# Performance work log

Measured on AMD Instinct MI355X. Metric: run time of the kernel, lower is better.

The kernel has to match this reference:

```python
import jax, jax.numpy as jnp
import numpy as np

NUM_ITERATIONS = 3


def squash(s, axis=-1):
    # s * sqrt(||s||^2) / (1 + ||s||^2), matching the torch source exactly
    sq = jnp.sum(s * s, axis=axis, keepdims=True)
    return s * jnp.sqrt(sq) / (1.0 + sq)


def setup_inputs() -> dict:
    key = jax.random.key(0)
    k_u, k_w = jax.random.split(key)
    B, J, R, O, I = 128, 166, 864, 8, 4
    u = jax.random.normal(k_u, (B, R, I), dtype=jnp.float32)
    W = jax.random.normal(k_w, (1, J, R, O, I), dtype=jnp.float32)
    return {"u": u, "W": W}


def reference(u, W):
    # u: [B, R, I]; W: [1, J, R, O, I]
    Wq = W[0]  # [J, R, O, I]
    # u_hat[b,j,r,o] = sum_i W[j,r,o,i] * u[b,r,i]
    u_hat = jnp.einsum('jroi,bri->bjro', Wq, u)  # [B, J, R, O]
    # routing logits start shared across batch (torch init: [1,J,R,1,1])
    b_ij = jnp.zeros((1, Wq.shape[0], Wq.shape[1]), dtype=u_hat.dtype)  # [1, J, R]
    v_j = None
    for it in range(NUM_ITERATIONS):
        c_ij = jax.nn.softmax(b_ij, axis=2)           # softmax over routes R
        s_j = jnp.einsum('bjr,bjro->bjo', jnp.broadcast_to(c_ij, u_hat.shape[:3]), u_hat)  # [B, J, O]
        v_j = squash(s_j, axis=-1)                    # [B, J, O]
        if it < NUM_ITERATIONS - 1:
            # agreement a[b,j,r] = <u_hat[b,j,r,:], v[b,j,:]>
            a_ij = jnp.einsum('bjro,bjo->bjr', u_hat, v_j)
            b_ij = b_ij + a_ij                        # broadcasts to [B, J, R]
    return v_j  # equivalent to torch v_j.squeeze() for B > 1
```

## Files before the change

### kernel.cpp

```cpp
#include <hip/hip_runtime.h>
#include <math.h>


#define BB 128
#define JJ 166
#define RR 864
#define OO 8
#define KMAX 14
#define RPAD2 257

typedef __fp16 h2v __attribute__((ext_vector_type(2)));

__device__ __forceinline__ uint32_t pack2(float a, float b) {
    return __builtin_bit_cast(uint32_t, __builtin_amdgcn_cvt_pkrtz(a, b));
}
__device__ __forceinline__ h2v bc_h2(uint32_t u) {
    return __builtin_bit_cast(h2v, u);
}
__device__ __forceinline__ float lo_f(uint32_t u) {
    return (float)__builtin_bit_cast(h2v, u).x;
}
__device__ __forceinline__ float hi_f(uint32_t u) {
    return (float)__builtin_bit_cast(h2v, u).y;
}

__device__ __forceinline__ float wave_sum(float v) {
#pragma unroll
    for (int m = 32; m >= 1; m >>= 1) v += __shfl_xor(v, m, 64);
    return v;
}

__global__ __launch_bounds__(256) void digitcaps_kernel(
    const float* __restrict__ u, const float* __restrict__ W,
    float* __restrict__ out) {
    const int tid = threadIdx.x;
    const int lane = tid & 63;
    const int wave = tid >> 6;

    const int j = blockIdx.x >> 5;
    const int b = ((blockIdx.x & 31) << 2) + wave;

    const float4* __restrict__ u4 = (const float4*)u;
    const float4* __restrict__ W4 = (const float4*)W;

    __shared__ uint2 wlds[2][OO * RPAD2];

    uint32_t uh[KMAX][4];

#define STAGE(CC, BUF, ITERS)                                                  \
    {                                                                          \
        const int gbase = j * (RR * OO) + (CC * 256) * OO;                     \
        _Pragma("unroll")                                                      \
        for (int i = 0; i < (ITERS); ++i) {                                    \
            const int e = tid + (i << 8);                                      \
            const float4 w = W4[gbase + e];                                    \
            wlds[BUF][(e & 7) * RPAD2 + (e >> 3)] =                            \
                make_uint2(pack2(w.x, w.y), pack2(w.z, w.w));                  \
        }                                                                      \
    }

#define COMPUTE(CC, BUF, KK)                                                   \
    {                                                                          \
        _Pragma("unroll")                                                      \
        for (int kl = 0; kl < (KK); ++kl) {                                    \
            const int rl = (kl << 6) + lane;                                   \
            const int r = (CC * 256) + rl;                                     \
            if (r < RR) {                      \
                const float4 uu = u4[b * RR + r];                              \
                const uint32_t up0 = pack2(uu.x, uu.y);                        \
                const uint32_t up1 = pack2(uu.z, uu.w);                        \
                float d[OO];                                                   \
                _Pragma("unroll")                                              \
                for (int o = 0; o < OO; ++o) {                                 \
                    const uint2 ww = wlds[BUF][o * RPAD2 + rl];                \
                    float t = __builtin_amdgcn_fdot2(bc_h2(ww.x), bc_h2(up0),  \
                                                     0.0f, false);             \
                    d[o] = __builtin_amdgcn_fdot2(bc_h2(ww.y), bc_h2(up1), t,  \
                                                  false);                      \
                }                                                              \
                _Pragma("unroll")                                              \
                for (int o2 = 0; o2 < 4; ++o2)                                 \
                    uh[(CC) * 4 + kl][o2] = pack2(d[2 * o2], d[2 * o2 + 1]);   \
            } else {                                                           \
                _Pragma("unroll")                                              \
                for (int o2 = 0; o2 < 4; ++o2) uh[(CC) * 4 + kl][o2] = 0u;     \
            }                                                                  \
        }                                                                      \
    }

    STAGE(0, 0, 8)
    __syncthreads();
    STAGE(1, 1, 8)
    COMPUTE(0, 0, 4)
    __syncthreads();
    STAGE(2, 0, 8)
    COMPUTE(1, 1, 4)
    __syncthreads();
    STAGE(3, 1, 3)
    COMPUTE(2, 0, 4)
    __syncthreads();
    COMPUTE(3, 1, 2)
#undef STAGE
#undef COMPUTE

    float V[OO];
    float v[OO];

    {
        h2v accp[4];
#pragma unroll
        for (int o2 = 0; o2 < 4; ++o2) accp[o2] = bc_h2(uh[0][o2]);
#pragma unroll
        for (int k = 1; k < KMAX; ++k)
#pragma unroll
            for (int o2 = 0; o2 < 4; ++o2) accp[o2] += bc_h2(uh[k][o2]);

        float s[OO];
#pragma unroll
        for (int o2 = 0; o2 < 4; ++o2) {
            s[2 * o2]     = wave_sum((float)accp[o2].x) * (1.0f / (float)RR);
            s[2 * o2 + 1] = wave_sum((float)accp[o2].y) * (1.0f / (float)RR);
        }
        float n2 = 0.0f;
#pragma unroll
        for (int o = 0; o < OO; ++o) n2 += s[o] * s[o];
        const float scale = sqrtf(n2) / (1.0f + n2);
#pragma unroll
        for (int o = 0; o < OO; ++o) { v[o] = s[o] * scale; V[o] = v[o]; }
    }

#pragma unroll
    for (int it = 1; it < 3; ++it) {
        uint32_t Vp[4];
#pragma unroll
        for (int o2 = 0; o2 < 4; ++o2)
            Vp[o2] = pack2(V[2 * o2], V[2 * o2 + 1]);

        float zp = 0.0f;
        float sp[OO];
#pragma unroll
        for (int o = 0; o < OO; ++o) sp[o] = 0.0f;

#pragma unroll
        for (int k = 0; k < KMAX; ++k) {
            float br = 0.0f;
#pragma unroll
            for (int o2 = 0; o2 < 4; ++o2)
                br = __builtin_amdgcn_fdot2(bc_h2(uh[k][o2]), bc_h2(Vp[o2]),
                                            br, false);
            const float e = (k < KMAX - 1 || lane < 32) ? __expf(br) : 0.0f;
            zp += e;
#pragma unroll
            for (int o2 = 0; o2 < 4; ++o2) {
                sp[2 * o2]     = fmaf(e, lo_f(uh[k][o2]), sp[2 * o2]);
                sp[2 * o2 + 1] = fmaf(e, hi_f(uh[k][o2]), sp[2 * o2 + 1]);
            }
        }
        const float invZ = 1.0f / wave_sum(zp);

        float s[OO];
#pragma unroll
        for (int o = 0; o < OO; ++o) s[o] = wave_sum(sp[o]) * invZ;

        float n2 = 0.0f;
#pragma unroll
        for (int o = 0; o < OO; ++o) n2 += s[o] * s[o];
        const float scale = sqrtf(n2) / (1.0f + n2);
#pragma unroll
        for (int o = 0; o < OO; ++o) v[o] = s[o] * scale;

        if (it < 2) {
#pragma unroll
            for (int o = 0; o < OO; ++o) V[o] += v[o];
        }
    }

    float outv = 0.0f;
#pragma unroll
    for (int o = 0; o < OO; ++o)
        if (lane == o) outv = v[o];
    if (lane < OO) out[(b * JJ + j) * OO + lane] = outv;
}

extern "C" void kernel_launch(void* const* d_in, const int* in_sizes, int n_in,
                              void* d_out, int out_size, void* d_ws, size_t ws_size,
                              hipStream_t stream) {
    const float* u = (const float*)d_in[0];
    const float* W = (const float*)d_in[1];
    float* out = (float*)d_out;

    const int grid = JJ * (BB / 4);
    digitcaps_kernel<<<grid, 256, 0, stream>>>(u, W, out);
}
```

Baseline: 144.0 us.

## Prepack W and u to fp16 in workspace and stream via global_load_lds

Adds a prepack kernel that converts W and u to packed fp16 in workspace, with W stored in an o-major, route-tiled layout and u padded. The main kernel then stages W tiles directly into LDS with global_load_lds, doing no per-block conversion or transpose. It also reads pre-packed u without bounds checks, moves to 512-thread blocks (8 batches per block), and remaps block IDs so neighbouring blocks share j. This removes the redundant per-block fp32 loads and conversions of W, which were repeated 32 times per j, at the cost of an extra kernel launch and a workspace round-trip.

```diff
diff --git a/kernel.cpp b/kernel.cpp
--- a/kernel.cpp
+++ b/kernel.cpp
@@ -7,7 +7,8 @@
 #define RR 864
 #define OO 8
 #define KMAX 14
-#define RPAD2 257
+#define WP_U2 (JJ * 7168)
+#define UP_U2 (BB * 896)
 
 typedef __fp16 h2v __attribute__((ext_vector_type(2)));
 
@@ -30,76 +31,111 @@
     return v;
 }
 
-__global__ __launch_bounds__(256) void digitcaps_kernel(
+__global__ __launch_bounds__(256) void prepack_kernel(
     const float* __restrict__ u, const float* __restrict__ W,
+    uint2* __restrict__ ws) {
+    const int t = threadIdx.x;
+    const int bid = blockIdx.x;
+    if (bid < JJ * 4) {
+        const int j = bid >> 2;
+        const int c = bid & 3;
+        const float4* __restrict__ W4 = (const float4*)W;
+        uint2* __restrict__ dst = ws + (size_t)j * 7168 + c * 2048;
+        if (c < 3) {
+#pragma unroll
+            for (int i = 0; i < 8; ++i) {
+                const int r = c * 256 + t;
+                const float4 w = W4[((size_t)j * RR + r) * 8 + i];
+                dst[i * 256 + t] = make_uint2(pack2(w.x, w.y), pack2(w.z, w.w));
+            }
+        } else {
+#pragma unroll
+            for (int i = 0; i < 4; ++i) {
+                const int e = i * 256 + t;
+                const int o = e >> 7;
+                const int rl = e & 127;
+                float4 w = make_float4(0.f, 0.f, 0.f, 0.f);
+                if (rl < 96) w = W4[((size_t)j * RR + 768 + rl) * 8 + o];
+                dst[e] = make_uint2(pack2(w.x, w.y), pack2(w.z, w.w));
+            }
+        }
+    } else {
+        const int e = (bid - JJ * 4) * 256 + t;
+        const int b = e / 896;
+        const int r = e - b * 896;
+        const float4* __restrict__ u4 = (const float4*)u;
+        float4 uu = make_float4(0.f, 0.f, 0.f, 0.f);
+        if (r < RR) uu = u4[(size_t)b * RR + r];
+        ws[WP_U2 + e] = make_uint2(pack2(uu.x, uu.y), pack2(uu.z, uu.w));
+    }
+}
+
+__global__ __launch_bounds__(512) void digitcaps_kernel(
+    const uint2* __restrict__ Wp, const uint2* __restrict__ uP,
     float* __restrict__ out) {
     const int tid = threadIdx.x;
     const int lane = tid & 63;
     const int wave = tid >> 6;
 
-    const int j = blockIdx.x >> 5;
-    const int b = ((blockIdx.x & 31) << 2) + wave;
-
-    const float4* __restrict__ u4 = (const float4*)u;
-    const float4* __restrict__ W4 = (const float4*)W;
-
-    __shared__ uint2 wlds[2][OO * RPAD2];
+    int bid = blockIdx.x;
+    bid = (bid & 7) * 332 + (bid >> 3);
+    const int j = bid >> 4;
+    const int b = ((bid & 15) << 3) + wave;
+
+    __shared__ uint2 wlds[2][2048];
+
+    const uint2* __restrict__ uPb = uP + (size_t)b * 896;
 
     uint32_t uh[KMAX][4];
 
-#define STAGE(CC, BUF, ITERS)                                                  \
+#define STAGE(CC, BUF, ROUNDS)                                                 \
     {                                                                          \
-        const int gbase = j * (RR * OO) + (CC * 256) * OO;                     \
+        const char* gsrc =                                                     \
+            (const char*)(Wp + (size_t)j * 7168 + (CC) * 2048);                \
         _Pragma("unroll")                                                      \
-        for (int i = 0; i < (ITERS); ++i) {                                    \
-            const int e = tid + (i << 8);                                      \
-            const float4 w = W4[gbase + e];                                    \
-            wlds[BUF][(e & 7) * RPAD2 + (e >> 3)] =                            \
-                make_uint2(pack2(w.x, w.y), pack2(w.z, w.w));                  \
+        for (int i = 0; i < (ROUNDS); ++i) {                                   \
+            __builtin_amdgcn_global_load_lds(                                  \
+                (const __attribute__((address_space(1))) uint32_t*)            \
+                    (gsrc + i * 8192 + tid * 16),                              \
+                (__attribute__((address_space(3))) uint32_t*)                  \
+                    ((char*)(&wlds[BUF][0]) + i * 8192 + (wave << 10)),        \
+                16, 0, 0);                                                     \
         }                                                                      \
     }
 
-#define COMPUTE(CC, BUF, KK)                                                   \
+#define COMPUTE(CC, BUF, KK, STRIDE)                                           \
     {                                                                          \
         _Pragma("unroll")                                                      \
         for (int kl = 0; kl < (KK); ++kl) {                                    \
             const int rl = (kl << 6) + lane;                                   \
-            const int r = (CC * 256) + rl;                                     \
-            if (r < RR) {                      \
-                const float4 uu = u4[b * RR + r];                              \
-                const uint32_t up0 = pack2(uu.x, uu.y);                        \
-                const uint32_t up1 = pack2(uu.z, uu.w);                        \
-                float d[OO];                                                   \
-                _Pragma("unroll")                                              \
-                for (int o = 0; o < OO; ++o) {                                 \
-                    const uint2 ww = wlds[BUF][o * RPAD2 + rl];                \
-                    float t = __builtin_amdgcn_fdot2(bc_h2(ww.x), bc_h2(up0),  \
-                                                     0.0f, false);             \
-                    d[o] = __builtin_amdgcn_fdot2(bc_h2(ww.y), bc_h2(up1), t,  \
-                                                  false);                      \
-                }                                                              \
-                _Pragma("unroll")                                              \
-                for (int o2 = 0; o2 < 4; ++o2)                                 \
-                    uh[(CC) * 4 + kl][o2] = pack2(d[2 * o2], d[2 * o2 + 1]);   \
-            } else {                                                           \
-                _Pragma("unroll")                                              \
-                for (int o2 = 0; o2 < 4; ++o2) uh[(CC) * 4 + kl][o2] = 0u;     \
+            const uint2 up = uPb[(CC) * 256 + rl];                             \
+            float d[OO];                                                       \
+            _Pragma("unroll")                                                  \
+            for (int o = 0; o < OO; ++o) {                                     \
+                const uint2 ww = wlds[BUF][o * (STRIDE) + rl];                 \
+                float t = __builtin_amdgcn_fdot2(bc_h2(ww.x), bc_h2(up.x),     \
+                                                 0.0f, false);                 \
+                d[o] = __builtin_amdgcn_fdot2(bc_h2(ww.y), bc_h2(up.y), t,     \
+                                              false);                          \
             }                                                                  \
+            _Pragma("unroll")                                                  \
+            for (int o2 = 0; o2 < 4; ++o2)                                     \
+                uh[(CC) * 4 + kl][o2] = pack2(d[2 * o2], d[2 * o2 + 1]);       \
         }                                                                      \
     }
 
-    STAGE(0, 0, 8)
-    __syncthreads();
-    STAGE(1, 1, 8)
-    COMPUTE(0, 0, 4)
-    __syncthreads();
-    STAGE(2, 0, 8)
-    COMPUTE(1, 1, 4)
-    __syncthreads();
-    STAGE(3, 1, 3)
-    COMPUTE(2, 0, 4)
-    __syncthreads();
-    COMPUTE(3, 1, 2)
+    STAGE(0, 0, 2)
+    __syncthreads();
+    STAGE(1, 1, 2)
+    COMPUTE(0, 0, 4, 256)
+    __syncthreads();
+    STAGE(2, 0, 2)
+    COMPUTE(1, 1, 4, 256)
+    __syncthreads();
+    STAGE(3, 1, 1)
+    COMPUTE(2, 0, 4, 256)
+    __syncthreads();
+    COMPUTE(3, 1, 2, 128)
 #undef STAGE
 #undef COMPUTE
 
@@ -188,7 +224,9 @@
     const float* u = (const float*)d_in[0];
     const float* W = (const float*)d_in[1];
     float* out = (float*)d_out;
-
-    const int grid = JJ * (BB / 4);
-    digitcaps_kernel<<<grid, 256, 0, stream>>>(u, W, out);
-}
+    uint2* ws = (uint2*)d_ws;
+
+    prepack_kernel<<<JJ * 4 + (BB * 896) / 256, 256, 0, stream>>>(u, W, ws);
+
+    digitcaps_kernel<<<JJ * 16, 512, 0, stream>>>(ws, ws + WP_U2, out);
+}
```

New measurement: 155.2 us. 7.8% more time.
